# Kernel optimization log

Measured on AMD Instinct MI355X. Metric: run time of the kernel, lower is better.

Reference implementation:

```python
import jax, jax.numpy as jnp
import numpy as np

EMB = 1024
HEADS = 16
HEAD_DIM = EMB // HEADS
DFF = 4 * EMB
EPS = 1e-5


def gelu_tanh(x):
    c = jnp.sqrt(jnp.asarray(2.0 / jnp.pi, dtype=x.dtype))
    return 0.5 * x * (1.0 + jnp.tanh(c * (x + 0.044715 * x ** 3)))


def layernorm(x, scale, shift):
    mean = jnp.mean(x, axis=-1, keepdims=True)
    var = jnp.mean((x - mean) ** 2, axis=-1, keepdims=True)
    return scale * ((x - mean) / jnp.sqrt(var + EPS)) + shift


def setup_inputs() -> dict:
    key = jax.random.key(0)
    ks = jax.random.split(key, 12)
    s = 0.02
    return {
        "x": jax.random.normal(ks[0], (2, 2048, EMB), dtype=jnp.float32),
        "Wq": jax.random.normal(ks[1], (EMB, EMB), dtype=jnp.float32) * s,
        "Wk": jax.random.normal(ks[2], (EMB, EMB), dtype=jnp.float32) * s,
        "Wv": jax.random.normal(ks[3], (EMB, EMB), dtype=jnp.float32) * s,
        "Wo": jax.random.normal(ks[4], (EMB, EMB), dtype=jnp.float32) * s,
        "bo": jnp.zeros((EMB,), dtype=jnp.float32),
        "W1": jax.random.normal(ks[5], (EMB, DFF), dtype=jnp.float32) * s,
        "b1": jnp.zeros((DFF,), dtype=jnp.float32),
        "W2": jax.random.normal(ks[6], (DFF, EMB), dtype=jnp.float32) * s,
        "b2": jnp.zeros((EMB,), dtype=jnp.float32),
        "g1": jnp.ones((EMB,), dtype=jnp.float32),
        "s1": jnp.zeros((EMB,), dtype=jnp.float32),
        "g2": jnp.ones((EMB,), dtype=jnp.float32),
        "s2": jnp.zeros((EMB,), dtype=jnp.float32),
    }


def reference(x, Wq, Wk, Wv, Wo, bo, W1, b1, W2, b2, g1, s1, g2, s2):
    B, S, E = x.shape
    # attention sub-block (pre-norm, residual)
    h = layernorm(x, g1, s1)
    Q = (h @ Wq).reshape(B, S, HEADS, HEAD_DIM)
    K = (h @ Wk).reshape(B, S, HEADS, HEAD_DIM)
    V = (h @ Wv).reshape(B, S, HEADS, HEAD_DIM)
    # scores: [B, H, S, S]
    scores = jnp.einsum("bqhd,bkhd->bhqk", Q, K)
    causal = jnp.tril(jnp.ones((S, S), dtype=bool))
    scores = jnp.where(causal, scores, -jnp.inf)
    attn = jax.nn.softmax(scores / np.sqrt(HEAD_DIM), axis=-1)
    ctx = jnp.einsum("bhqk,bkhd->bqhd", attn, V).reshape(B, S, E)
    x = x + (ctx @ Wo + bo)
    # FFN sub-block
    h = layernorm(x, g2, s2)
    h = gelu_tanh(h @ W1 + b1) @ W2 + b2
    return x + h
```

## Files before the change

kernel.cpp:

```cpp
#include <hip/hip_runtime.h>
#include <hip/hip_bf16.h>

typedef __attribute__((ext_vector_type(8))) short short8;
typedef __attribute__((ext_vector_type(4))) float f32x4;

#define EMB   1024
#define DFF   4096
#define S_LEN 2048
#define NB    2
#define MTOT  (NB * S_LEN)
#define HEADS 16
#define HDIM  64
#define QKN   2048

__device__ __forceinline__ float bf2f(unsigned short u) {
  return __uint_as_float(((unsigned int)u) << 16);
}
__device__ __forceinline__ unsigned short f2bf(float f) {
  unsigned int x = __float_as_uint(f);
  unsigned int r = (x + 0x7fffu + ((x >> 16) & 1u)) >> 16;
  return (unsigned short)r;
}
__device__ __forceinline__ unsigned int cvtpk(float a, float b) {
  unsigned int r;
  asm("v_cvt_pk_bf16_f32 %0, %1, %2" : "=v"(r) : "v"(a), "v"(b));
  return r;
}

__device__ __forceinline__ void gl_lds16(const unsigned short* g, unsigned short* l) {
  __builtin_amdgcn_global_load_lds(
      (const __attribute__((address_space(1))) unsigned int*)g,
      (__attribute__((address_space(3))) unsigned int*)l, 16, 0, 0);
}

__device__ __forceinline__ float gelu_tanh_f(float v) {
  float u = v + 0.044715f * v * v * v;
  float t = tanhf(0.7978845608028654f * u);
  return 0.5f * v * (1.0f + t);
}

__global__ __launch_bounds__(256) void fused_transpose(
    const float* __restrict__ Wq, const float* __restrict__ Wk,
    const float* __restrict__ Wv, const float* __restrict__ Wo,
    const float* __restrict__ W1, const float* __restrict__ W2,
    unsigned short* __restrict__ wtQ, unsigned short* __restrict__ wtK,
    unsigned short* __restrict__ wtV, unsigned short* __restrict__ wtO,
    unsigned short* __restrict__ wtW1, unsigned short* __restrict__ wtW2)
{
  __shared__ float t[64][33];
  const int bid = (int)blockIdx.x;
  const float* W; unsigned short* Wt; int K, N, local;
  if (bid < 2048) {
    const int sel = bid >> 9; local = bid & 511; K = 1024; N = 1024;
    W  = sel == 0 ? Wq  : sel == 1 ? Wk  : sel == 2 ? Wv  : Wo;
    Wt = sel == 0 ? wtQ : sel == 1 ? wtK : sel == 2 ? wtV : wtO;
  } else if (bid < 4096) {
    local = bid - 2048; K = 1024; N = 4096; W = W1; Wt = wtW1;
  } else {
    local = bid - 4096; K = 4096; N = 1024; W = W2; Wt = wtW2;
  }
  const int nbx = N >> 5;
  const int n0 = (local % nbx) * 32, k0 = (local / nbx) * 64;
  const int tx = threadIdx.x, ty = threadIdx.y;
#pragma unroll
  for (int i = 0; i < 8; ++i) {
    const int kr = i * 8 + ty;
    t[kr][tx] = W[(size_t)(k0 + kr) * N + n0 + tx];
  }
  __syncthreads();
#pragma unroll
  for (int i = 0; i < 4; ++i) {
    const int r = ty + i * 8;
    const unsigned int u = cvtpk(t[2 * tx][r], t[2 * tx + 1][r]);
    *(unsigned int*)(&Wt[(size_t)(n0 + r) * K + k0 + 2 * tx]) = u;
  }
}

__global__ __launch_bounds__(256) void ln_kernel(
    const float* __restrict__ X, const float* __restrict__ g,
    const float* __restrict__ sh, unsigned short* __restrict__ H)
{
  const int row = blockIdx.x, t = threadIdx.x;
  const float* xr = X + (size_t)row * EMB;
  float4 v = *(const float4*)(xr + t * 4);
  float s  = v.x + v.y + v.z + v.w;
  float ss = v.x * v.x + v.y * v.y + v.z * v.z + v.w * v.w;
#pragma unroll
  for (int off = 32; off > 0; off >>= 1) {
    s  += __shfl_xor(s, off);
    ss += __shfl_xor(ss, off);
  }
  __shared__ float rs[4], rss[4];
  const int wid = t >> 6;
  if ((t & 63) == 0) { rs[wid] = s; rss[wid] = ss; }
  __syncthreads();
  s  = rs[0] + rs[1] + rs[2] + rs[3];
  ss = rss[0] + rss[1] + rss[2] + rss[3];
  const float mean = s * (1.f / EMB);
  const float var  = ss * (1.f / EMB) - mean * mean;
  const float rstd = rsqrtf(var + 1e-5f);
  float4 gv = *(const float4*)(g + t * 4);
  float4 sv = *(const float4*)(sh + t * 4);
  ushort4 o;
  o.x = f2bf((v.x - mean) * rstd * gv.x + sv.x);
  o.y = f2bf((v.y - mean) * rstd * gv.y + sv.y);
  o.z = f2bf((v.z - mean) * rstd * gv.z + sv.z);
  o.w = f2bf((v.w - mean) * rstd * gv.w + sv.w);
  *(ushort4*)(H + (size_t)row * EMB + t * 4) = o;
}

__global__ __launch_bounds__(512, 2) void gemm256(
    const unsigned short* __restrict__ A, const unsigned short* __restrict__ Bt,
    const float* __restrict__ bias, unsigned short* __restrict__ outb)
{
  __shared__ unsigned short As[2][256 * 64];
  __shared__ unsigned short Bs[2][256 * 64];

  const int tid = threadIdx.x;
  const int lane = tid & 63, wid = tid >> 6;
  const int bid = (int)blockIdx.x;
  const int swz = (bid & 7) * 32 + (bid >> 3);
  const int by = swz >> 4, bx = swz & 15;
  const int m0 = by * 256, n0 = bx * 256;
  const int wr = wid >> 2, wc = wid & 3;
  const int l16 = lane & 15, kg = lane >> 4;

  const int sr  = lane >> 3;
  const int scs = ((lane & 7) ^ (lane >> 3)) * 8;
  const int rx  = l16 & 7;

  const unsigned short* Abase = A + (size_t)m0 * 1024;
  const unsigned short* Bbase = Bt + (size_t)n0 * 1024;

  f32x4 acc[8][4];
#pragma unroll
  for (int i = 0; i < 8; ++i)
#pragma unroll
    for (int j = 0; j < 4; ++j) acc[i][j] = (f32x4){0.f, 0.f, 0.f, 0.f};

#define STG256(buf, t)                                                         \
  do {                                                                         \
    const int k0_ = (t) * 64;                                                  \
    _Pragma("unroll")                                                          \
    for (int i_ = 0; i_ < 4; ++i_) {                                           \
      const int ca_ = wid * 4 + i_;                                            \
      gl_lds16(Abase + (size_t)(ca_ * 8 + sr) * 1024 + k0_ + scs,              \
               &As[buf][ca_ * 512]);                                           \
      gl_lds16(Bbase + (size_t)(ca_ * 8 + sr) * 1024 + k0_ + scs,              \
               &Bs[buf][ca_ * 512]);                                           \
    }                                                                          \
  } while (0)

  STG256(0, 0);
  asm volatile("s_waitcnt vmcnt(0)" ::: "memory");
  __builtin_amdgcn_s_barrier();

  const int nt = 1024 / 64;
  for (int t = 0; t < nt; ++t) {
    const int b = t & 1;
    if (t + 1 < nt) STG256(b ^ 1, t + 1);
#pragma unroll
    for (int kk = 0; kk < 2; ++kk) {
      short8 af[8];
#pragma unroll
      for (int i = 0; i < 8; ++i) {
        const int row = wr * 128 + i * 16 + l16;
        af[i] = *(const short8*)(&As[b][row * 64 + ((kg + kk * 4) ^ rx) * 8]);
      }
      __builtin_amdgcn_s_setprio(1);
#pragma unroll
      for (int j = 0; j < 4; ++j) {
        const int row = wc * 64 + j * 16 + l16;
        short8 bf = *(const short8*)(&Bs[b][row * 64 + ((kg + kk * 4) ^ rx) * 8]);
#pragma unroll
        for (int i = 0; i < 8; ++i)
          acc[i][j] = __builtin_amdgcn_mfma_f32_16x16x32_bf16(af[i], bf, acc[i][j], 0, 0, 0);
      }
      __builtin_amdgcn_s_setprio(0);
    }
    asm volatile("s_waitcnt lgkmcnt(0)" ::: "memory");
    asm volatile("s_waitcnt vmcnt(0)" ::: "memory");
    __builtin_amdgcn_s_barrier();
  }
#undef STG256

#pragma unroll
  for (int i = 0; i < 8; ++i) {
#pragma unroll
    for (int j = 0; j < 4; ++j) {
      const int c = n0 + wc * 64 + j * 16 + l16;
      const float bc = bias[c];
#pragma unroll
      for (int r = 0; r < 4; ++r) {
        const int row = m0 + wr * 128 + i * 16 + kg * 4 + r;
        outb[(size_t)row * 4096 + c] = f2bf(gelu_tanh_f(acc[i][j][r] + bc));
      }
    }
  }
}

template <int MODE, int BN, int BKT, int NBUF>
__global__ __launch_bounds__(256, 2) void gemm_gl(
    const unsigned short* __restrict__ A, const unsigned short* __restrict__ Bt,
    int M, int N, int Kloop, int Kld, int nbx,
    const float* __restrict__ bias, const float* __restrict__ resf,
    float* __restrict__ outf, unsigned short* __restrict__ outb,
    unsigned short* __restrict__ vt)
{
  constexpr int NFRAG = BN / 32;
  constexpr int KK    = BKT / 32;
  constexpr int ACH   = 128 * BKT / 512;
  constexpr int BCH   = BN  * BKT / 512;
  __shared__ unsigned short As[NBUF][128 * BKT];
  __shared__ unsigned short Bs[NBUF][BN * BKT];

  const int tid = threadIdx.x;
  const int lane = tid & 63, wid = tid >> 6;
  const int nwg = (int)gridDim.x;
  const int cpx = nwg >> 3;
  const int bid = (int)blockIdx.x;
  const int swz = (bid & 7) * cpx + (bid >> 3);
  const int by = swz / nbx;
  const int bx = swz - by * nbx;
  const int m0 = by * 128, n0 = bx * BN;
  const int wr = wid >> 1, wc = wid & 1;
  const int l16 = lane & 15, kg = lane >> 4;

  int sr, scs;
  if constexpr (BKT == 32) {
    sr  = lane >> 2;
    scs = ((lane & 3) ^ ((lane >> 3) & 3)) * 8;
  } else {
    sr  = lane >> 3;
    scs = ((lane & 7) ^ (lane >> 3)) * 8;
  }
  const int rx = (BKT == 32) ? ((l16 >> 1) & 3) : (l16 & 7);

  const unsigned short* Abase = A + (size_t)m0 * Kld;
  const unsigned short* Bbase = Bt + (size_t)n0 * Kld;

  f32x4 acc[4][NFRAG];
#pragma unroll
  for (int i = 0; i < 4; ++i)
#pragma unroll
    for (int j = 0; j < NFRAG; ++j) acc[i][j] = (f32x4){0.f, 0.f, 0.f, 0.f};

  const int nt = Kloop / BKT;
  constexpr int RPC = (BKT == 32) ? 16 : 8;

#define STAGE(buf, t)                                                          \
  do {                                                                         \
    const int k0_ = (t) * BKT;                                                 \
    _Pragma("unroll")                                                          \
    for (int i_ = 0; i_ < ACH / 4; ++i_) {                                     \
      const int chunk_ = wid * (ACH / 4) + i_;                                 \
      gl_lds16(Abase + (size_t)(chunk_ * RPC + sr) * Kld + k0_ + scs,          \
               &As[buf][0] + chunk_ * 512);                                    \
    }                                                                          \
    _Pragma("unroll")                                                          \
    for (int i_ = 0; i_ < BCH / 4; ++i_) {                                     \
      const int chunk_ = wid * (BCH / 4) + i_;                                 \
      gl_lds16(Bbase + (size_t)(chunk_ * RPC + sr) * Kld + k0_ + scs,          \
               &Bs[buf][0] + chunk_ * 512);                                    \
    }                                                                          \
  } while (0)

#define VM_WAIT()                                                              \
  do {                                                                         \
    constexpr int W_ = ((ACH + BCH) / 4) * (NBUF - 1);                         \
    if constexpr (W_ == 3)      asm volatile("s_waitcnt vmcnt(3)" ::: "memory"); \
    else if constexpr (W_ == 4) asm volatile("s_waitcnt vmcnt(4)" ::: "memory"); \
    else if constexpr (W_ == 6) asm volatile("s_waitcnt vmcnt(6)" ::: "memory"); \
    else if constexpr (W_ == 8) asm volatile("s_waitcnt vmcnt(8)" ::: "memory"); \
    else                        asm volatile("s_waitcnt vmcnt(12)" ::: "memory"); \
  } while (0)

  STAGE(0, 0);
  STAGE(1, 1);
  if constexpr (NBUF == 3) STAGE(2, 2);
  VM_WAIT();
  __builtin_amdgcn_s_barrier();

  int b = 0;
  for (int t = 0; t < nt; ++t) {
    short8 af[4][KK], bfr[NFRAG][KK];
#pragma unroll
    for (int i = 0; i < 4; ++i)
#pragma unroll
      for (int kk = 0; kk < KK; ++kk)
        af[i][kk] = *(const short8*)(
            &As[b][(wr * 64 + i * 16 + l16) * BKT + ((kg + kk * 4) ^ rx) * 8]);
#pragma unroll
    for (int j = 0; j < NFRAG; ++j)
#pragma unroll
      for (int kk = 0; kk < KK; ++kk)
        bfr[j][kk] = *(const short8*)(
            &Bs[b][(wc * (BN / 2) + j * 16 + l16) * BKT + ((kg + kk * 4) ^ rx) * 8]);
#pragma unroll
    for (int kk = 0; kk < KK; ++kk)
#pragma unroll
      for (int i = 0; i < 4; ++i)
#pragma unroll
        for (int j = 0; j < NFRAG; ++j)
          acc[i][j] = __builtin_amdgcn_mfma_f32_16x16x32_bf16(af[i][kk], bfr[j][kk], acc[i][j], 0, 0, 0);
    asm volatile("s_waitcnt lgkmcnt(0)" ::: "memory");
    __builtin_amdgcn_s_barrier();
    if (t + NBUF < nt) {
      STAGE(b, t + NBUF);
      VM_WAIT();
    } else {
      asm volatile("s_waitcnt vmcnt(0)" ::: "memory");
    }
    __builtin_amdgcn_s_barrier();
    if constexpr (NBUF == 2) b ^= 1;
    else                     b = (b == 2) ? 0 : b + 1;
  }
#undef STAGE
#undef VM_WAIT

#pragma unroll
  for (int i = 0; i < 4; ++i) {
#pragma unroll
    for (int j = 0; j < NFRAG; ++j) {
      const int c = n0 + wc * (BN / 2) + j * 16 + l16;
      if constexpr (MODE == 0) {
        if (c >= 2048) {
          const int row0 = m0 + wr * 64 + i * 16 + kg * 4;
          const int dcol = c - 2048;
          ushort4 w4;
          w4.x = f2bf(acc[i][j][0]); w4.y = f2bf(acc[i][j][1]);
          w4.z = f2bf(acc[i][j][2]); w4.w = f2bf(acc[i][j][3]);
          *(ushort4*)(&vt[((size_t)((row0 >> 11) * 16 + (dcol >> 6)) * 64 +
                           (dcol & 63)) * 2048 + (row0 & 2047)]) = w4;
        } else {
          const float sc = (c < 1024) ? 0.18033688011112042f : 1.0f;
#pragma unroll
          for (int r = 0; r < 4; ++r) {
            const int row = m0 + wr * 64 + i * 16 + kg * 4 + r;
            outb[(size_t)row * QKN + c] = f2bf(acc[i][j][r] * sc);
          }
        }
      } else {
#pragma unroll
        for (int r = 0; r < 4; ++r) {
          const int row = m0 + wr * 64 + i * 16 + kg * 4 + r;
          const size_t idx = (size_t)row * N + c;
          float v = acc[i][j][r];
          if constexpr (MODE == 1) {
            outf[idx] = v + bias[c] + resf[idx];
          } else if constexpr (MODE == 2) {
            outb[idx] = f2bf(gelu_tanh_f(v + bias[c]));
          } else {
            outf[idx] = v + bias[c] + resf[idx];
          }
        }
      }
    }
  }
}

__global__ __launch_bounds__(256) void attn_mfma(
    const unsigned short* __restrict__ qkv, const unsigned short* __restrict__ Vt,
    unsigned short* __restrict__ ctx)
{
  __shared__ unsigned short Ks[64][64];
  __shared__ unsigned short Vs[64][64];
  __shared__ unsigned short Ps[4][2][16][64];

  const int tid  = threadIdx.x;
  const int lane = tid & 63, wv = tid >> 6;
  const int l16  = lane & 15, kg = lane >> 4;
  const int bid  = (int)blockIdx.x;
  const int swz  = (bid & 7) * 64 + (bid >> 3);
  const int pair = swz & 15;
  const int bh   = swz >> 4;
  const int b    = bh >> 4, h = bh & 15;
  const int qtg0 = pair;
  const int qtg1 = 31 - pair;

  const size_t qbase  = ((size_t)b * S_LEN) * QKN + h * HDIM;
  const size_t kbase  = qbase + 1024;
  const size_t vtbase = ((size_t)bh * HDIM) * S_LEN;
  const size_t cbase  = ((size_t)b * S_LEN) * EMB + h * HDIM;

  short8 qf[2][2];
#pragma unroll
  for (int g = 0; g < 2; ++g) {
    const int qt = g ? qtg1 : qtg0;
    const unsigned short* qrow =
        qkv + qbase + (size_t)(qt * 64 + wv * 16 + l16) * QKN;
    qf[g][0] = *(const short8*)(qrow + kg * 8);
    qf[g][1] = *(const short8*)(qrow + 32 + kg * 8);
  }

  f32x4 o[2][4];
#pragma unroll
  for (int g = 0; g < 2; ++g)
#pragma unroll
    for (int dt = 0; dt < 4; ++dt) o[g][dt] = (f32x4){0.f, 0.f, 0.f, 0.f};
  float m[2] = {-1e30f, -1e30f}, l[2] = {0.f, 0.f};

  const int srow = tid >> 2;
  const int c0   = tid & 3;
  const int sx   = srow & 7;
  const int col0 = ((2 * c0)     ^ sx) * 8;
  const int col1 = ((2 * c0 + 1) ^ sx) * 8;
  const int rx   = l16 & 7;
  const int ntiles = qtg1 + 1;

  const unsigned short* ksrc = qkv + kbase + (size_t)srow * QKN + c0 * 16;
  const unsigned short* vsrc = Vt + vtbase + (size_t)srow * S_LEN + c0 * 16;
  short8 k0 = *(const short8*)(ksrc);
  short8 k1 = *(const short8*)(ksrc + 8);
  short8 v0 = *(const short8*)(vsrc);
  short8 v1 = *(const short8*)(vsrc + 8);

  for (int kt = 0; kt < ntiles; ++kt) {
    __syncthreads();
    *(short8*)(&Ks[srow][col0]) = k0;
    *(short8*)(&Ks[srow][col1]) = k1;
    *(short8*)(&Vs[srow][col0]) = v0;
    *(short8*)(&Vs[srow][col1]) = v1;
    __syncthreads();

    if (kt + 1 < ntiles) {
      const unsigned short* kn =
          qkv + kbase + (size_t)((kt + 1) * 64 + srow) * QKN + c0 * 16;
      const unsigned short* vn =
          Vt + vtbase + (size_t)srow * S_LEN + (kt + 1) * 64 + c0 * 16;
      k0 = *(const short8*)(kn);
      k1 = *(const short8*)(kn + 8);
      v0 = *(const short8*)(vn);
      v1 = *(const short8*)(vn + 8);
    }

    const bool act0 = (kt <= qtg0);

    short8 kf0[4], kf1[4];
#pragma unroll
    for (int j = 0; j < 4; ++j) {
      kf0[j] = *(const short8*)(&Ks[j * 16 + l16][(kg ^ rx) * 8]);
      kf1[j] = *(const short8*)(&Ks[j * 16 + l16][((kg + 4) ^ rx) * 8]);
    }

    float fac[2] = {1.f, 1.f};
    bool resc[2] = {false, false};
#pragma unroll
    for (int g = 0; g < 2; ++g) {
      if (g == 0 && !act0) continue;
      const int qt = g ? qtg1 : qtg0;

      f32x4 sa[4];
      __builtin_amdgcn_s_setprio(1);
#pragma unroll
      for (int j = 0; j < 4; ++j) {
        sa[j] = (f32x4){0.f, 0.f, 0.f, 0.f};
        sa[j] = __builtin_amdgcn_mfma_f32_16x16x32_bf16(kf0[j], qf[g][0], sa[j], 0, 0, 0);
        sa[j] = __builtin_amdgcn_mfma_f32_16x16x32_bf16(kf1[j], qf[g][1], sa[j], 0, 0, 0);
      }
      __builtin_amdgcn_s_setprio(0);

      if (kt == qt) {
        const int qloc = wv * 16 + l16;
#pragma unroll
        for (int j = 0; j < 4; ++j)
#pragma unroll
          for (int r = 0; r < 4; ++r)
            if (j * 16 + kg * 4 + r > qloc) sa[j][r] = -1e30f;
      }

      float m0j = fmaxf(fmaxf(sa[0][0], sa[0][1]), fmaxf(sa[0][2], sa[0][3]));
      float m1j = fmaxf(fmaxf(sa[1][0], sa[1][1]), fmaxf(sa[1][2], sa[1][3]));
      float m2j = fmaxf(fmaxf(sa[2][0], sa[2][1]), fmaxf(sa[2][2], sa[2][3]));
      float m3j = fmaxf(fmaxf(sa[3][0], sa[3][1]), fmaxf(sa[3][2], sa[3][3]));
      float mx = fmaxf(fmaxf(m0j, m1j), fmaxf(m2j, m3j));
      mx = fmaxf(mx, __shfl_xor(mx, 16));
      mx = fmaxf(mx, __shfl_xor(mx, 32));
      if (!__all(mx - m[g] <= 8.0f)) {
        const float mn = fmaxf(m[g], mx);
        fac[g] = exp2f(m[g] - mn);
        m[g] = mn;
        resc[g] = true;
      }
      const float mcur = m[g];
      float ps = 0.f;
#pragma unroll
      for (int j = 0; j < 4; ++j) {
        float p0 = exp2f(sa[j][0] - mcur);
        float p1 = exp2f(sa[j][1] - mcur);
        float p2 = exp2f(sa[j][2] - mcur);
        float p3 = exp2f(sa[j][3] - mcur);
        sa[j][0] = p0; sa[j][1] = p1; sa[j][2] = p2; sa[j][3] = p3;
        ps += (p0 + p1) + (p2 + p3);
      }
      ps += __shfl_xor(ps, 16);
      ps += __shfl_xor(ps, 32);
      l[g] = l[g] * fac[g] + ps;

#pragma unroll
      for (int j = 0; j < 4; ++j) {
        uint2 pw;
        pw.x = cvtpk(sa[j][0], sa[j][1]);
        pw.y = cvtpk(sa[j][2], sa[j][3]);
        *(uint2*)(&Ps[wv][g][l16][((2 * j + (kg >> 1)) ^ rx) * 8 + (kg & 1) * 4]) = pw;
      }
    }

#pragma unroll
    for (int g = 0; g < 2; ++g) {
      if (resc[g]) {
#pragma unroll
        for (int dt = 0; dt < 4; ++dt)
#pragma unroll
          for (int r = 0; r < 4; ++r) o[g][dt][r] *= fac[g];
      }
    }

    short8 pf[2][2];
#pragma unroll
    for (int g = 0; g < 2; ++g) {
      if (g == 0 && !act0) continue;
      pf[g][0] = *(const short8*)(&Ps[wv][g][l16][(kg ^ rx) * 8]);
      pf[g][1] = *(const short8*)(&Ps[wv][g][l16][((kg + 4) ^ rx) * 8]);
    }
    __builtin_amdgcn_s_setprio(1);
#pragma unroll
    for (int dt = 0; dt < 4; ++dt) {
      short8 vf0 = *(const short8*)(&Vs[dt * 16 + l16][(kg ^ rx) * 8]);
      short8 vf1 = *(const short8*)(&Vs[dt * 16 + l16][((kg + 4) ^ rx) * 8]);
#pragma unroll
      for (int g = 0; g < 2; ++g) {
        if (g == 0 && !act0) continue;
        o[g][dt] = __builtin_amdgcn_mfma_f32_16x16x32_bf16(vf0, pf[g][0], o[g][dt], 0, 0, 0);
        o[g][dt] = __builtin_amdgcn_mfma_f32_16x16x32_bf16(vf1, pf[g][1], o[g][dt], 0, 0, 0);
      }
    }
    __builtin_amdgcn_s_setprio(0);
  }

#pragma unroll
  for (int g = 0; g < 2; ++g) {
    const int qt = g ? qtg1 : qtg0;
    const float inv = 1.0f / l[g];
    const int qrow = qt * 64 + wv * 16 + l16;
#pragma unroll
    for (int dt = 0; dt < 4; ++dt) {
      uint2 cw;
      cw.x = cvtpk(o[g][dt][0] * inv, o[g][dt][1] * inv);
      cw.y = cvtpk(o[g][dt][2] * inv, o[g][dt][3] * inv);
      *(uint2*)(&ctx[cbase + (size_t)qrow * EMB + dt * 16 + kg * 4]) = cw;
    }
  }
}

extern "C" void kernel_launch(void* const* d_in, const int* in_sizes, int n_in,
                              void* d_out, int out_size, void* d_ws, size_t ws_size,
                              hipStream_t stream)
{
  const float* x  = (const float*)d_in[0];
  const float* Wq = (const float*)d_in[1];
  const float* Wk = (const float*)d_in[2];
  const float* Wv = (const float*)d_in[3];
  const float* Wo = (const float*)d_in[4];
  const float* bo = (const float*)d_in[5];
  const float* W1 = (const float*)d_in[6];
  const float* b1 = (const float*)d_in[7];
  const float* W2 = (const float*)d_in[8];
  const float* b2 = (const float*)d_in[9];
  const float* g1 = (const float*)d_in[10];
  const float* s1 = (const float*)d_in[11];
  const float* g2 = (const float*)d_in[12];
  const float* s2 = (const float*)d_in[13];

  float* out = (float*)d_out;
  char* ws = (char*)d_ws;
  const size_t MB = 1024 * 1024;
  unsigned short* wtQ  = (unsigned short*)(ws + 0 * MB);
  unsigned short* wtK  = (unsigned short*)(ws + 2 * MB);
  unsigned short* wtV  = (unsigned short*)(ws + 4 * MB);
  unsigned short* wtO  = (unsigned short*)(ws + 6 * MB);
  unsigned short* wtW1 = (unsigned short*)(ws + 8 * MB);
  unsigned short* wtW2 = (unsigned short*)(ws + 16 * MB);
  unsigned short* h    = (unsigned short*)(ws + 24 * MB);
  unsigned short* qkv  = (unsigned short*)(ws + 32 * MB);
  unsigned short* Vt   = (unsigned short*)(ws + 56 * MB);
  unsigned short* ctxb = h;
  unsigned short* h2   = h;
  unsigned short* gbuf = qkv;

  fused_transpose<<<dim3(6144), dim3(32, 8), 0, stream>>>(
      Wq, Wk, Wv, Wo, W1, W2, wtQ, wtK, wtV, wtO, wtW1, wtW2);

  ln_kernel<<<MTOT, 256, 0, stream>>>(x, g1, s1, h);

  gemm_gl<0, 128, 32, 2><<<dim3(24 * 32), 256, 0, stream>>>(
      h, wtQ, MTOT, 3072, 1024, 1024, 24, nullptr, nullptr, nullptr, qkv, Vt);

  attn_mfma<<<dim3(512), 256, 0, stream>>>(qkv, Vt, ctxb);

  gemm_gl<1, 64, 64, 2><<<dim3(16 * 32), 256, 0, stream>>>(
      ctxb, wtO, MTOT, 1024, 1024, 1024, 16, bo, x, out, nullptr, nullptr);

  ln_kernel<<<MTOT, 256, 0, stream>>>(out, g2, s2, h2);

  gemm256<<<dim3(256), 512, 0, stream>>>(h2, wtW1, b1, gbuf);

  gemm_gl<3, 64, 64, 2><<<dim3(16 * 32), 256, 0, stream>>>(
      gbuf, wtW2, MTOT, 1024, DFF, DFF, 16, b2, out, out, nullptr, nullptr);
}
```

Measured before the change: 235.9 us.

## Double attention key/value tile to 128 keys per iteration

The causal attention kernel now stages 128 keys per loop iteration instead of 64. K is held as a 128x64 shared tile and V^T as a 64x128 tile, each with an XOR swizzle, and each thread prefetches 32 elements per row. The score, softmax and PV loops are widened to cover the larger tile, which halves the number of barrier-separated iterations and online-softmax rescale checks. The cost is more LDS and register use per block, and extra masked work on diagonal tiles, where half of a 128-wide tile can be wasted.

```diff
diff --git a/kernel.cpp b/kernel.cpp
--- a/kernel.cpp
+++ b/kernel.cpp
@@ -363,9 +363,9 @@
     const unsigned short* __restrict__ qkv, const unsigned short* __restrict__ Vt,
     unsigned short* __restrict__ ctx)
 {
-  __shared__ unsigned short Ks[64][64];
-  __shared__ unsigned short Vs[64][64];
-  __shared__ unsigned short Ps[4][2][16][64];
+  __shared__ unsigned short Ks[128][64];
+  __shared__ unsigned short Vs[64][128];
+  __shared__ unsigned short Ps[4][2][16][128];
 
   const int tid  = threadIdx.x;
   const int lane = tid & 63, wv = tid >> 6;
@@ -400,48 +400,53 @@
     for (int dt = 0; dt < 4; ++dt) o[g][dt] = (f32x4){0.f, 0.f, 0.f, 0.f};
   float m[2] = {-1e30f, -1e30f}, l[2] = {0.f, 0.f};
 
-  const int srow = tid >> 2;
-  const int c0   = tid & 3;
-  const int sx   = srow & 7;
-  const int col0 = ((2 * c0)     ^ sx) * 8;
-  const int col1 = ((2 * c0 + 1) ^ sx) * 8;
-  const int rx   = l16 & 7;
-  const int ntiles = qtg1 + 1;
-
-  const unsigned short* ksrc = qkv + kbase + (size_t)srow * QKN + c0 * 16;
-  const unsigned short* vsrc = Vt + vtbase + (size_t)srow * S_LEN + c0 * 16;
-  short8 k0 = *(const short8*)(ksrc);
-  short8 k1 = *(const short8*)(ksrc + 8);
-  short8 v0 = *(const short8*)(vsrc);
-  short8 v1 = *(const short8*)(vsrc + 8);
-
-  for (int kt = 0; kt < ntiles; ++kt) {
+  const int kr2 = tid >> 1, kh = tid & 1;
+  const int ksx = kr2 & 7;
+  const int vr = tid >> 2, vc = tid & 3;
+  const int vsx = vr & 7;
+  const int rx = l16 & 7;
+
+  const int nkt = (qtg1 + 2) >> 1;
+
+  const unsigned short* ksrc = qkv + kbase + (size_t)kr2 * QKN + kh * 32;
+  const unsigned short* vsrc = Vt + vtbase + (size_t)vr * S_LEN + vc * 32;
+  short8 kv0 = *(const short8*)(ksrc);
+  short8 kv1 = *(const short8*)(ksrc + 8);
+  short8 kv2 = *(const short8*)(ksrc + 16);
+  short8 kv3 = *(const short8*)(ksrc + 24);
+  short8 vv0 = *(const short8*)(vsrc);
+  short8 vv1 = *(const short8*)(vsrc + 8);
+  short8 vv2 = *(const short8*)(vsrc + 16);
+  short8 vv3 = *(const short8*)(vsrc + 24);
+
+  for (int kt = 0; kt < nkt; ++kt) {
     __syncthreads();
-    *(short8*)(&Ks[srow][col0]) = k0;
-    *(short8*)(&Ks[srow][col1]) = k1;
-    *(short8*)(&Vs[srow][col0]) = v0;
-    *(short8*)(&Vs[srow][col1]) = v1;
+    *(short8*)(&Ks[kr2][((kh * 4 + 0) ^ ksx) * 8]) = kv0;
+    *(short8*)(&Ks[kr2][((kh * 4 + 1) ^ ksx) * 8]) = kv1;
+    *(short8*)(&Ks[kr2][((kh * 4 + 2) ^ ksx) * 8]) = kv2;
+    *(short8*)(&Ks[kr2][((kh * 4 + 3) ^ ksx) * 8]) = kv3;
+    *(short8*)(&Vs[vr][((vc * 4 + 0) ^ vsx) * 8]) = vv0;
+    *(short8*)(&Vs[vr][((vc * 4 + 1) ^ vsx) * 8]) = vv1;
+    *(short8*)(&Vs[vr][((vc * 4 + 2) ^ vsx) * 8]) = vv2;
+    *(short8*)(&Vs[vr][((vc * 4 + 3) ^ vsx) * 8]) = vv3;
     __syncthreads();
 
-    if (kt + 1 < ntiles) {
+    if (kt + 1 < nkt) {
       const unsigned short* kn =
-          qkv + kbase + (size_t)((kt + 1) * 64 + srow) * QKN + c0 * 16;
+          qkv + kbase + (size_t)((kt + 1) * 128 + kr2) * QKN + kh * 32;
       const unsigned short* vn =
-          Vt + vtbase + (size_t)srow * S_LEN + (kt + 1) * 64 + c0 * 16;
-      k0 = *(const short8*)(kn);
-      k1 = *(const short8*)(kn + 8);
-      v0 = *(const short8*)(vn);
-      v1 = *(const short8*)(vn + 8);
-    }
-
-    const bool act0 = (kt <= qtg0);
-
-    short8 kf0[4], kf1[4];
-#pragma unroll
-    for (int j = 0; j < 4; ++j) {
-      kf0[j] = *(const short8*)(&Ks[j * 16 + l16][(kg ^ rx) * 8]);
-      kf1[j] = *(const short8*)(&Ks[j * 16 + l16][((kg + 4) ^ rx) * 8]);
-    }
+          Vt + vtbase + (size_t)vr * S_LEN + (kt + 1) * 128 + vc * 32;
+      kv0 = *(const short8*)(kn);
+      kv1 = *(const short8*)(kn + 8);
+      kv2 = *(const short8*)(kn + 16);
+      kv3 = *(const short8*)(kn + 24);
+      vv0 = *(const short8*)(vn);
+      vv1 = *(const short8*)(vn + 8);
+      vv2 = *(const short8*)(vn + 16);
+      vv3 = *(const short8*)(vn + 24);
+    }
+
+    const bool act0 = (2 * kt <= qtg0);
 
     float fac[2] = {1.f, 1.f};
     bool resc[2] = {false, false};
@@ -450,30 +455,33 @@
       if (g == 0 && !act0) continue;
       const int qt = g ? qtg1 : qtg0;
 
-      f32x4 sa[4];
+      f32x4 sa[8];
       __builtin_amdgcn_s_setprio(1);
 #pragma unroll
-      for (int j = 0; j < 4; ++j) {
+      for (int j = 0; j < 8; ++j) {
+        short8 kf0 = *(const short8*)(&Ks[j * 16 + l16][(kg ^ rx) * 8]);
+        short8 kf1 = *(const short8*)(&Ks[j * 16 + l16][((kg + 4) ^ rx) * 8]);
         sa[j] = (f32x4){0.f, 0.f, 0.f, 0.f};
-        sa[j] = __builtin_amdgcn_mfma_f32_16x16x32_bf16(kf0[j], qf[g][0], sa[j], 0, 0, 0);
-        sa[j] = __builtin_amdgcn_mfma_f32_16x16x32_bf16(kf1[j], qf[g][1], sa[j], 0, 0, 0);
+        sa[j] = __builtin_amdgcn_mfma_f32_16x16x32_bf16(kf0, qf[g][0], sa[j], 0, 0, 0);
+        sa[j] = __builtin_amdgcn_mfma_f32_16x16x32_bf16(kf1, qf[g][1], sa[j], 0, 0, 0);
       }
       __builtin_amdgcn_s_setprio(0);
 
-      if (kt == qt) {
-        const int qloc = wv * 16 + l16;
-#pragma unroll
-        for (int j = 0; j < 4; ++j)
+      const int qloc = qt * 64 + wv * 16 + l16;
+      if (kt * 128 + 127 > qt * 64 + wv * 16) {
+#pragma unroll
+        for (int j = 0; j < 8; ++j)
 #pragma unroll
           for (int r = 0; r < 4; ++r)
-            if (j * 16 + kg * 4 + r > qloc) sa[j][r] = -1e30f;
-      }
-
-      float m0j = fmaxf(fmaxf(sa[0][0], sa[0][1]), fmaxf(sa[0][2], sa[0][3]));
-      float m1j = fmaxf(fmaxf(sa[1][0], sa[1][1]), fmaxf(sa[1][2], sa[1][3]));
-      float m2j = fmaxf(fmaxf(sa[2][0], sa[2][1]), fmaxf(sa[2][2], sa[2][3]));
-      float m3j = fmaxf(fmaxf(sa[3][0], sa[3][1]), fmaxf(sa[3][2], sa[3][3]));
-      float mx = fmaxf(fmaxf(m0j, m1j), fmaxf(m2j, m3j));
+            if (kt * 128 + j * 16 + kg * 4 + r > qloc) sa[j][r] = -1e30f;
+      }
+
+      float mx = fmaxf(fmaxf(sa[0][0], sa[0][1]), fmaxf(sa[0][2], sa[0][3]));
+#pragma unroll
+      for (int j = 1; j < 8; ++j) {
+        float mj = fmaxf(fmaxf(sa[j][0], sa[j][1]), fmaxf(sa[j][2], sa[j][3]));
+        mx = fmaxf(mx, mj);
+      }
       mx = fmaxf(mx, __shfl_xor(mx, 16));
       mx = fmaxf(mx, __shfl_xor(mx, 32));
       if (!__all(mx - m[g] <= 8.0f)) {
@@ -485,7 +493,7 @@
       const float mcur = m[g];
       float ps = 0.f;
 #pragma unroll
-      for (int j = 0; j < 4; ++j) {
+      for (int j = 0; j < 8; ++j) {
         float p0 = exp2f(sa[j][0] - mcur);
         float p1 = exp2f(sa[j][1] - mcur);
         float p2 = exp2f(sa[j][2] - mcur);
@@ -498,7 +506,7 @@
       l[g] = l[g] * fac[g] + ps;
 
 #pragma unroll
-      for (int j = 0; j < 4; ++j) {
+      for (int j = 0; j < 8; ++j) {
         uint2 pw;
         pw.x = cvtpk(sa[j][0], sa[j][1]);
         pw.y = cvtpk(sa[j][2], sa[j][3]);
@@ -516,23 +524,25 @@
       }
     }
 
-    short8 pf[2][2];
+    short8 pf[2][4];
 #pragma unroll
     for (int g = 0; g < 2; ++g) {
       if (g == 0 && !act0) continue;
-      pf[g][0] = *(const short8*)(&Ps[wv][g][l16][(kg ^ rx) * 8]);
-      pf[g][1] = *(const short8*)(&Ps[wv][g][l16][((kg + 4) ^ rx) * 8]);
+#pragma unroll
+      for (int s = 0; s < 4; ++s)
+        pf[g][s] = *(const short8*)(&Ps[wv][g][l16][((4 * s + kg) ^ rx) * 8]);
     }
     __builtin_amdgcn_s_setprio(1);
 #pragma unroll
     for (int dt = 0; dt < 4; ++dt) {
-      short8 vf0 = *(const short8*)(&Vs[dt * 16 + l16][(kg ^ rx) * 8]);
-      short8 vf1 = *(const short8*)(&Vs[dt * 16 + l16][((kg + 4) ^ rx) * 8]);
-#pragma unroll
-      for (int g = 0; g < 2; ++g) {
-        if (g == 0 && !act0) continue;
-        o[g][dt] = __builtin_amdgcn_mfma_f32_16x16x32_bf16(vf0, pf[g][0], o[g][dt], 0, 0, 0);
-        o[g][dt] = __builtin_amdgcn_mfma_f32_16x16x32_bf16(vf1, pf[g][1], o[g][dt], 0, 0, 0);
+#pragma unroll
+      for (int s = 0; s < 4; ++s) {
+        short8 vf = *(const short8*)(&Vs[dt * 16 + l16][((4 * s + kg) ^ rx) * 8]);
+#pragma unroll
+        for (int g = 0; g < 2; ++g) {
+          if (g == 0 && !act0) continue;
+          o[g][dt] = __builtin_amdgcn_mfma_f32_16x16x32_bf16(vf, pf[g][s], o[g][dt], 0, 0, 0);
+        }
       }
     }
     __builtin_amdgcn_s_setprio(0);
```

Measured after the change: 237.6 us. No clear change (+0.7%).
